# Performance work log

Hardware: AMD Instinct MI355X
Metric: run time of the kernel (lower is better)

The kernel has to match this reference:

```python
import jax, jax.numpy as jnp
import numpy as np

NX, NC = 8192, 8192
X_DIM, C_DIM, H_DIM, K_DIM, Y_DIM = 3, 3, 512, 512, 3
N_LAYERS = 4
ACTIVATION = 'sigmoid'


def _init_mlp(key, in_dim, h_dim, out_dim, n_layers):
    ks = jax.random.split(key, 3)
    W0 = jax.random.normal(ks[0], (in_dim, h_dim), jnp.float32) / np.sqrt(in_dim)
    b0 = jnp.zeros((h_dim,), jnp.float32)
    Wh = jax.random.normal(ks[1], (n_layers - 1, h_dim, h_dim), jnp.float32) / np.sqrt(h_dim)
    bh = jnp.zeros((n_layers - 1, h_dim), jnp.float32)
    Wo = jax.random.normal(ks[2], (h_dim, out_dim), jnp.float32) / np.sqrt(h_dim)
    bo = jnp.zeros((out_dim,), jnp.float32)
    return W0, b0, Wh, bh, Wo, bo


def _mlp(x, W0, b0, Wh, bh, Wo, bo):
    # SIREN-style MLP (BaseNet with x_scale=alpha=gamma=1)
    h = jnp.sin(x @ W0 + b0)
    for i in range(Wh.shape[0]):  # fixed small n_layers-1 loop
        h = jnp.sin(h @ Wh[i] + bh[i])
    return h @ Wo + bo


def setup_inputs() -> dict:
    key = jax.random.key(0)
    kx, kc, kq, kk, kv = jax.random.split(key, 5)
    inp = {
        'x': jax.random.normal(kx, (NX, X_DIM), jnp.float32),
        'c': jax.random.normal(kc, (NC, C_DIM), jnp.float32),
    }
    for name, k, in_dim, out_dim in (('Q', kq, X_DIM, K_DIM), ('K', kk, C_DIM, K_DIM), ('V', kv, C_DIM, Y_DIM)):
        W0, b0, Wh, bh, Wo, bo = _init_mlp(k, in_dim, H_DIM, out_dim, N_LAYERS)
        inp[f'{name}W0'], inp[f'{name}b0'] = W0, b0
        inp[f'{name}Wh'], inp[f'{name}bh'] = Wh, bh
        inp[f'{name}Wo'], inp[f'{name}bo'] = Wo, bo
    return inp


def reference(x, c, QW0, Qb0, QWh, Qbh, QWo, Qbo,
              KW0, Kb0, KWh, Kbh, KWo, Kbo,
              VW0, Vb0, VWh, Vbh, VWo, Vbo):
    Q = _mlp(x, QW0, Qb0, QWh, Qbh, QWo, Qbo)   # [Nx, k_dim]
    K = _mlp(c, KW0, Kb0, KWh, Kbh, KWo, Kbo)   # [Nc, k_dim]
    V = _mlp(c, VW0, Vb0, VWh, Vbh, VWo, Vbo)   # [Nc, y_dim]
    A = Q @ K.T                                  # [Nx, Nc]
    if ACTIVATION == 'sigmoid':
        A = jax.nn.sigmoid(A)
    elif ACTIVATION == 'softplus':
        A = jax.nn.softplus(A)
    elif ACTIVATION == 'softmax':
        A = jax.nn.softmax(A, axis=1)
    return A @ V                                 # [Nx, y_dim]
```

## Files before the change

### kernel.cpp

```cpp
#include <hip/hip_runtime.h>
#include <math.h>

#define NXR 8192
#define NCR 8192
#define HD  512
#define NSL 16
#define JC  (NCR / NSL)
#define KSTR 520

typedef short s16x8 __attribute__((ext_vector_type(8)));
typedef float f32x4 __attribute__((ext_vector_type(4)));
typedef unsigned short u16;

struct P11 { const float* p[11]; };
struct P3  { const float* p[3]; };

__device__ inline u16 f2bf(float f) {
    unsigned int u = __float_as_uint(f);
    u = (u + 0x7FFFu + ((u >> 16) & 1u)) >> 16;
    return (u16)u;
}
__device__ inline float bf2f(u16 h) {
    return __uint_as_float(((unsigned int)h) << 16);
}

__global__ __launch_bounds__(256) void transpose_w_all(
    P11 srcs, u16* __restrict__ out)
{
    const float* in = srcs.p[blockIdx.z];
    u16* o = out + (size_t)blockIdx.z * HD * HD;
    __shared__ float tile[32][33];
    int bx = blockIdx.x * 32, by = blockIdx.y * 32;
    int tx = threadIdx.x & 31, ty = threadIdx.x >> 5;
    for (int r = ty; r < 32; r += 8)
        tile[r][tx] = in[(size_t)(by + r) * HD + bx + tx];
    __syncthreads();
    for (int r = ty; r < 32; r += 8)
        o[(size_t)(bx + r) * HD + by + tx] = f2bf(tile[tx][r]);
}

__global__ __launch_bounds__(256) void layer0_all(
    const float* __restrict__ x, const float* __restrict__ c,
    P3 W0p, P3 b0p, u16* __restrict__ H, int net_base)
{
    int z = blockIdx.z;
    int net = net_base + z;
    const float* X  = (net == 0) ? x : c;
    const float* W0 = W0p.p[z];
    const float* b0 = b0p.p[z];
    u16* Hn = H + (size_t)z * NXR * HD;

    int idx = (blockIdx.x * 256 + threadIdx.x) * 8;
    int n = idx & (HD - 1);
    int row = idx >> 9;
    float x0 = X[row * 3 + 0], x1 = X[row * 3 + 1], x2 = X[row * 3 + 2];
    s16x8 o;
#pragma unroll
    for (int j = 0; j < 8; ++j) {
        float v = x0 * W0[n + j] + x1 * W0[HD + n + j] + x2 * W0[2 * HD + n + j] + b0[n + j];
        ((u16*)&o)[j] = f2bf(__sinf(v));
    }
    *(s16x8*)&Hn[idx] = o;
}

template<int ACT>
__global__ __launch_bounds__(256) void gemm_rs(
    const u16* __restrict__ Abase, const u16* __restrict__ Wt0, size_t wstride,
    P3 bias, u16* __restrict__ Cbase)
{
    __shared__ u16 Ws[32 * KSTR];

    const int net = blockIdx.z;
    const u16* A  = Abase + (size_t)net * NXR * HD;
    const u16* Wt = Wt0 + (size_t)net * wstride;
    const float* bias_p = bias.p[net];
    u16* C = Cbase + (size_t)net * NXR * HD;

    const int tid = threadIdx.x;
    const int wave = tid >> 6, lane = tid & 63;
    const int row0 = blockIdx.x * 128;
    const int colbase = blockIdx.y * 128;

    const int qm = lane & 15;
    const int g  = lane >> 4;

    s16x8 qf[16][2];
    {
        const u16* ap = A + (size_t)(row0 + wave * 32 + qm) * HD + g * 8;
#pragma unroll
        for (int t = 0; t < 16; ++t) {
            qf[t][0] = *(const s16x8*)(ap + t * 32);
            qf[t][1] = *(const s16x8*)(ap + (size_t)16 * HD + t * 32);
        }
    }

    for (int ct = 0; ct < 4; ++ct) {
        const int col0 = colbase + ct * 32;

#pragma unroll
        for (int i = 0; i < 8; ++i) {
            int chunk = i * 256 + tid;
            int cc = chunk >> 6;
            int ch = chunk & 63;
            s16x8 v = *(const s16x8*)(Wt + (size_t)(col0 + cc) * HD + ch * 8);
            *(s16x8*)&Ws[cc * KSTR + ch * 8] = v;
        }
        __syncthreads();

        f32x4 acc[2][2] = {};
#pragma unroll
        for (int kt = 0; kt < 16; ++kt) {
            s16x8 b0 = *(const s16x8*)&Ws[qm * KSTR + kt * 32 + g * 8];
            s16x8 b1 = *(const s16x8*)&Ws[(16 + qm) * KSTR + kt * 32 + g * 8];
            acc[0][0] = __builtin_amdgcn_mfma_f32_16x16x32_bf16(qf[kt][0], b0, acc[0][0], 0, 0, 0);
            acc[0][1] = __builtin_amdgcn_mfma_f32_16x16x32_bf16(qf[kt][0], b1, acc[0][1], 0, 0, 0);
            acc[1][0] = __builtin_amdgcn_mfma_f32_16x16x32_bf16(qf[kt][1], b0, acc[1][0], 0, 0, 0);
            acc[1][1] = __builtin_amdgcn_mfma_f32_16x16x32_bf16(qf[kt][1], b1, acc[1][1], 0, 0, 0);
        }

        float bv0 = bias_p[col0 + qm];
        float bv1 = bias_p[col0 + 16 + qm];
#pragma unroll
        for (int h = 0; h < 2; ++h) {
#pragma unroll
            for (int r = 0; r < 4; ++r) {
                int grow = row0 + wave * 32 + h * 16 + g * 4 + r;
                float v0 = acc[h][0][r] + bv0;
                float v1 = acc[h][1][r] + bv1;
                if (ACT) { v0 = __sinf(v0); v1 = __sinf(v1); }
                C[(size_t)grow * HD + col0 + qm]      = f2bf(v0);
                C[(size_t)grow * HD + col0 + 16 + qm] = f2bf(v1);
            }
        }
        __syncthreads();
    }
}

__global__ __launch_bounds__(256) void vout_k(
    const u16* __restrict__ H, const float* __restrict__ Wo,
    const float* __restrict__ bo, float* __restrict__ V)
{
    int wave = threadIdx.x >> 6, lane = threadIdx.x & 63;
    int row = blockIdx.x * 4 + wave;
    s16x8 hv = *(const s16x8*)(H + (size_t)row * HD + lane * 8);
    float a0 = 0, a1 = 0, a2 = 0;
#pragma unroll
    for (int j = 0; j < 8; ++j) {
        float hf = bf2f(((const u16*)&hv)[j]);
        int k = lane * 8 + j;
        a0 += hf * Wo[k * 3 + 0];
        a1 += hf * Wo[k * 3 + 1];
        a2 += hf * Wo[k * 3 + 2];
    }
#pragma unroll
    for (int d = 32; d >= 1; d >>= 1) {
        a0 += __shfl_down(a0, d);
        a1 += __shfl_down(a1, d);
        a2 += __shfl_down(a2, d);
    }
    if (lane == 0) {
        V[row * 3 + 0] = a0 + bo[0];
        V[row * 3 + 1] = a1 + bo[1];
        V[row * 3 + 2] = a2 + bo[2];
    }
}

__global__ __launch_bounds__(256) void attn_mfma(
    const u16* __restrict__ Q, const u16* __restrict__ K,
    const float* __restrict__ V, float* __restrict__ out)
{
    __shared__ u16 Ks[32 * KSTR];

    const int tid = threadIdx.x;
    const int wave = tid >> 6, lane = tid & 63;
    const int row0 = blockIdx.y * 128;
    const int col_base = blockIdx.x * JC;

    const int qm = lane & 15;
    const int g  = lane >> 4;

    s16x8 qf[16][2];
    {
        const u16* qp = Q + (size_t)(row0 + wave * 32 + qm) * HD + g * 8;
#pragma unroll
        for (int t = 0; t < 16; ++t) {
            qf[t][0] = *(const s16x8*)(qp + t * 32);
            qf[t][1] = *(const s16x8*)(qp + (size_t)16 * HD + t * 32);
        }
    }

    float po[2][4][3] = {};

    for (int jt = 0; jt < JC / 32; ++jt) {
        const int col0 = col_base + jt * 32;

#pragma unroll
        for (int i = 0; i < 8; ++i) {
            int chunk = i * 256 + tid;
            int cc = chunk >> 6;
            int ch = chunk & 63;
            s16x8 v = *(const s16x8*)(K + (size_t)(col0 + cc) * HD + ch * 8);
            *(s16x8*)&Ks[cc * KSTR + ch * 8] = v;
        }
        __syncthreads();

        float vv[2][3];
#pragma unroll
        for (int ct = 0; ct < 2; ++ct) {
            size_t vr = (size_t)(col0 + ct * 16 + qm) * 3;
            vv[ct][0] = V[vr + 0];
            vv[ct][1] = V[vr + 1];
            vv[ct][2] = V[vr + 2];
        }

        f32x4 acc[2][2] = {};
#pragma unroll
        for (int kt = 0; kt < 16; ++kt) {
            s16x8 b0 = *(const s16x8*)&Ks[qm * KSTR + kt * 32 + g * 8];
            s16x8 b1 = *(const s16x8*)&Ks[(16 + qm) * KSTR + kt * 32 + g * 8];
            acc[0][0] = __builtin_amdgcn_mfma_f32_16x16x32_bf16(qf[kt][0], b0, acc[0][0], 0, 0, 0);
            acc[0][1] = __builtin_amdgcn_mfma_f32_16x16x32_bf16(qf[kt][0], b1, acc[0][1], 0, 0, 0);
            acc[1][0] = __builtin_amdgcn_mfma_f32_16x16x32_bf16(qf[kt][1], b0, acc[1][0], 0, 0, 0);
            acc[1][1] = __builtin_amdgcn_mfma_f32_16x16x32_bf16(qf[kt][1], b1, acc[1][1], 0, 0, 0);
        }

#pragma unroll
        for (int h = 0; h < 2; ++h)
#pragma unroll
            for (int ct = 0; ct < 2; ++ct)
#pragma unroll
                for (int r = 0; r < 4; ++r) {
                    float s = __builtin_amdgcn_rcpf(1.f + __expf(-acc[h][ct][r]));
                    po[h][r][0] += s * vv[ct][0];
                    po[h][r][1] += s * vv[ct][1];
                    po[h][r][2] += s * vv[ct][2];
                }
        __syncthreads();
    }

#pragma unroll
    for (int h = 0; h < 2; ++h)
#pragma unroll
        for (int r = 0; r < 4; ++r)
#pragma unroll
            for (int c = 0; c < 3; ++c) {
                float v = po[h][r][c];
                v += __shfl_down(v, 8, 16);
                v += __shfl_down(v, 4, 16);
                v += __shfl_down(v, 2, 16);
                v += __shfl_down(v, 1, 16);
                if (qm == 0)
                    atomicAdd(&out[(size_t)(row0 + wave * 32 + h * 16 + g * 4 + r) * 3 + c], v);
            }
}

extern "C" void kernel_launch(void* const* d_in, const int* in_sizes, int n_in,
                              void* d_out, int out_size, void* d_ws, size_t ws_size,
                              hipStream_t stream)
{
    const float* x   = (const float*)d_in[0];
    const float* c   = (const float*)d_in[1];
    const float* QW0 = (const float*)d_in[2];
    const float* Qb0 = (const float*)d_in[3];
    const float* QWh = (const float*)d_in[4];
    const float* Qbh = (const float*)d_in[5];
    const float* QWo = (const float*)d_in[6];
    const float* Qbo = (const float*)d_in[7];
    const float* KW0 = (const float*)d_in[8];
    const float* Kb0 = (const float*)d_in[9];
    const float* KWh = (const float*)d_in[10];
    const float* Kbh = (const float*)d_in[11];
    const float* KWo = (const float*)d_in[12];
    const float* Kbo = (const float*)d_in[13];
    const float* VW0 = (const float*)d_in[14];
    const float* Vb0 = (const float*)d_in[15];
    const float* VWh = (const float*)d_in[16];
    const float* Vbh = (const float*)d_in[17];
    const float* VWo = (const float*)d_in[18];
    const float* Vbo = (const float*)d_in[19];

    char* ws = (char*)d_ws;
    const size_t WTN = (size_t)HD * HD;
    const size_t MB = 1048576;
    const size_t NET = (size_t)NXR * HD;

    u16* wT = (u16*)ws;
    P11 tsrc;
    for (int l = 0; l < 3; ++l) {
        tsrc.p[l * 3 + 0] = QWh + (size_t)l * WTN;
        tsrc.p[l * 3 + 1] = KWh + (size_t)l * WTN;
        tsrc.p[l * 3 + 2] = VWh + (size_t)l * WTN;
    }
    tsrc.p[9]  = QWo;
    tsrc.p[10] = KWo;
    transpose_w_all<<<dim3(16, 16, 11), 256, 0, stream>>>(tsrc, wT);

    const int L0G = NXR * HD / 2048;
    const u16* Qb; const u16* Kb; const float* Vf;

    if (ws_size >= 57 * MB) {
        u16*   hA = (u16*)(ws + 6 * MB);
        u16*   hB = (u16*)(ws + 30 * MB);
        float* Vff = (float*)(ws + 54 * MB);

        P3 w0 = {{QW0, KW0, VW0}}, b0 = {{Qb0, Kb0, Vb0}};
        layer0_all<<<dim3(L0G, 1, 3), 256, 0, stream>>>(x, c, w0, b0, hA, 0);

        dim3 g3(NXR / 128, HD / 128, 3);
        {
            P3 b = {{Qbh + 0 * HD, Kbh + 0 * HD, Vbh + 0 * HD}};
            gemm_rs<1><<<g3, 256, 0, stream>>>(hA, wT + 0 * 3 * WTN, WTN, b, hB);
        }
        {
            P3 b = {{Qbh + 1 * HD, Kbh + 1 * HD, Vbh + 1 * HD}};
            gemm_rs<1><<<g3, 256, 0, stream>>>(hB, wT + 1 * 3 * WTN, WTN, b, hA);
        }
        {
            P3 b = {{Qbh + 2 * HD, Kbh + 2 * HD, Vbh + 2 * HD}};
            gemm_rs<1><<<g3, 256, 0, stream>>>(hA, wT + 2 * 3 * WTN, WTN, b, hB);
        }
        {
            P3 b = {{Qbo, Kbo, nullptr}};
            gemm_rs<0><<<dim3(NXR / 128, HD / 128, 2), 256, 0, stream>>>(
                hB, wT + 9 * WTN, WTN, b, hA);
        }
        vout_k<<<NCR / 4, 256, 0, stream>>>(hB + 2 * NET, VWo, Vbo, Vff);

        Qb = hA; Kb = hA + NET; Vf = Vff;
    } else {
        u16*   R1 = (u16*)(ws + 6 * MB);
        u16*   R2 = (u16*)(ws + 22 * MB);
        float* Vff = (float*)(ws + 38 * MB);

        {
            P3 w0 = {{VW0, nullptr, nullptr}}, b0 = {{Vb0, nullptr, nullptr}};
            layer0_all<<<dim3(L0G, 1, 1), 256, 0, stream>>>(x, c, w0, b0, R1, 2);
        }
        dim3 gv(NXR / 128, HD / 128, 1);
        {
            P3 b = {{Vbh + 0 * HD, nullptr, nullptr}};
            gemm_rs<1><<<gv, 256, 0, stream>>>(R1, wT + (0 * 3 + 2) * WTN, 0, b, R2);
        }
        {
            P3 b = {{Vbh + 1 * HD, nullptr, nullptr}};
            gemm_rs<1><<<gv, 256, 0, stream>>>(R2, wT + (1 * 3 + 2) * WTN, 0, b, R1);
        }
        {
            P3 b = {{Vbh + 2 * HD, nullptr, nullptr}};
            gemm_rs<1><<<gv, 256, 0, stream>>>(R1, wT + (2 * 3 + 2) * WTN, 0, b, R2);
        }
        vout_k<<<NCR / 4, 256, 0, stream>>>(R2, VWo, Vbo, Vff);

        {
            P3 w0 = {{QW0, KW0, nullptr}}, b0 = {{Qb0, Kb0, nullptr}};
            layer0_all<<<dim3(L0G, 1, 2), 256, 0, stream>>>(x, c, w0, b0, R1, 0);
        }
        dim3 gqk(NXR / 128, HD / 128, 2);
        {
            P3 b = {{Qbh + 0 * HD, Kbh + 0 * HD, nullptr}};
            gemm_rs<1><<<gqk, 256, 0, stream>>>(R1, wT + 0 * 3 * WTN, WTN, b, R2);
        }
        {
            P3 b = {{Qbh + 1 * HD, Kbh + 1 * HD, nullptr}};
            gemm_rs<1><<<gqk, 256, 0, stream>>>(R2, wT + 1 * 3 * WTN, WTN, b, R1);
        }
        {
            P3 b = {{Qbh + 2 * HD, Kbh + 2 * HD, nullptr}};
            gemm_rs<1><<<gqk, 256, 0, stream>>>(R1, wT + 2 * 3 * WTN, WTN, b, R2);
        }
        {
            P3 b = {{Qbo, Kbo, nullptr}};
            gemm_rs<0><<<gqk, 256, 0, stream>>>(R2, wT + 9 * WTN, WTN, b, R1);
        }
        Qb = R1; Kb = R1 + NET; Vf = Vff;
    }

    hipMemsetAsync(d_out, 0, (size_t)out_size * sizeof(float), stream);
    attn_mfma<<<dim3(NSL, NXR / 128), 256, 0, stream>>>(Qb, Kb, Vf, (float*)d_out);
}
```

Measured before the change: 306.3 us.

## Register-prefetch next weight/K tile and halve attention column slices

Both the MLP GEMM and the attention kernel now load the next 32-column tile of weights or K into registers while the MFMA loop runs on the current tile held in shared memory. The barrier placement is reorganised so there is one barrier before the shared-memory store and one after it, which hides global-load latency behind compute. NSL drops from 16 to 8, giving each attention block twice as many columns and halving the number of atomic adds, at the cost of fewer blocks in the grid. The prefetch adds 8 vector registers per thread on top of the already large qf fragment array, which risks lower occupancy or register spills.

```diff
diff --git a/kernel.cpp b/kernel.cpp
--- a/kernel.cpp
+++ b/kernel.cpp
@@ -4,7 +4,7 @@
 #define NXR 8192
 #define NCR 8192
 #define HD  512
-#define NSL 16
+#define NSL 8
 #define JC  (NCR / NSL)
 #define KSTR 520
 
@@ -84,6 +84,13 @@
     const int qm = lane & 15;
     const int g  = lane >> 4;
 
+    s16x8 pre[8];
+#pragma unroll
+    for (int i = 0; i < 8; ++i) {
+        int chunk = i * 256 + tid;
+        pre[i] = *(const s16x8*)(Wt + (size_t)(colbase + (chunk >> 6)) * HD + (chunk & 63) * 8);
+    }
+
     s16x8 qf[16][2];
     {
         const u16* ap = A + (size_t)(row0 + wave * 32 + qm) * HD + g * 8;
@@ -97,15 +104,22 @@
     for (int ct = 0; ct < 4; ++ct) {
         const int col0 = colbase + ct * 32;
 
+        __syncthreads();
 #pragma unroll
         for (int i = 0; i < 8; ++i) {
             int chunk = i * 256 + tid;
-            int cc = chunk >> 6;
-            int ch = chunk & 63;
-            s16x8 v = *(const s16x8*)(Wt + (size_t)(col0 + cc) * HD + ch * 8);
-            *(s16x8*)&Ws[cc * KSTR + ch * 8] = v;
+            *(s16x8*)&Ws[(chunk >> 6) * KSTR + (chunk & 63) * 8] = pre[i];
         }
         __syncthreads();
+
+        if (ct + 1 < 4) {
+            const int ncol = colbase + (ct + 1) * 32;
+#pragma unroll
+            for (int i = 0; i < 8; ++i) {
+                int chunk = i * 256 + tid;
+                pre[i] = *(const s16x8*)(Wt + (size_t)(ncol + (chunk >> 6)) * HD + (chunk & 63) * 8);
+            }
+        }
 
         f32x4 acc[2][2] = {};
 #pragma unroll
@@ -132,7 +146,6 @@
                 C[(size_t)grow * HD + col0 + 16 + qm] = f2bf(v1);
             }
         }
-        __syncthreads();
     }
 }
 
@@ -179,6 +192,13 @@
     const int qm = lane & 15;
     const int g  = lane >> 4;
 
+    s16x8 pre[8];
+#pragma unroll
+    for (int i = 0; i < 8; ++i) {
+        int chunk = i * 256 + tid;
+        pre[i] = *(const s16x8*)(K + (size_t)(col_base + (chunk >> 6)) * HD + (chunk & 63) * 8);
+    }
+
     s16x8 qf[16][2];
     {
         const u16* qp = Q + (size_t)(row0 + wave * 32 + qm) * HD + g * 8;
@@ -194,15 +214,22 @@
     for (int jt = 0; jt < JC / 32; ++jt) {
         const int col0 = col_base + jt * 32;
 
+        __syncthreads();
 #pragma unroll
         for (int i = 0; i < 8; ++i) {
             int chunk = i * 256 + tid;
-            int cc = chunk >> 6;
-            int ch = chunk & 63;
-            s16x8 v = *(const s16x8*)(K + (size_t)(col0 + cc) * HD + ch * 8);
-            *(s16x8*)&Ks[cc * KSTR + ch * 8] = v;
+            *(s16x8*)&Ks[(chunk >> 6) * KSTR + (chunk & 63) * 8] = pre[i];
         }
         __syncthreads();
+
+        if (jt + 1 < JC / 32) {
+            const int ncol = col_base + (jt + 1) * 32;
+#pragma unroll
+            for (int i = 0; i < 8; ++i) {
+                int chunk = i * 256 + tid;
+                pre[i] = *(const s16x8*)(K + (size_t)(ncol + (chunk >> 6)) * HD + (chunk & 63) * 8);
+            }
+        }
 
         float vv[2][3];
 #pragma unroll
@@ -235,7 +262,6 @@
                     po[h][r][1] += s * vv[ct][1];
                     po[h][r][2] += s * vv[ct][2];
                 }
-        __syncthreads();
     }
 
 #pragma unroll
```

Measured after the change: 293.3 us. 4.2% less time.

## Fuse hidden MLP layers and V projection into one persistent in-place kernel

Applied to the files above, without the earlier changes.

Replaces the per-layer gemm_rs launches and the separate vout_k kernel with a single mlp_mega kernel. Each block owns a 128-row strip of one network and runs every hidden layer in place, reloading its rows from global memory between layers. The V network's final 3-wide projection is done inside the same kernel. The attention column split (NSL) is also halved and the low-workspace fallback path is dropped. This saves launches and inter-kernel round trips, but cuts the MLP grid from 768 to 192 blocks, so each block does far more serial work and fewer CUs may be busy.

```diff
diff --git a/kernel.cpp b/kernel.cpp
--- a/kernel.cpp
+++ b/kernel.cpp
@@ -4,7 +4,7 @@
 #define NXR 8192
 #define NCR 8192
 #define HD  512
-#define NSL 16
+#define NSL 8
 #define JC  (NCR / NSL)
 #define KSTR 520
 
@@ -14,6 +14,7 @@
 
 struct P11 { const float* p[11]; };
 struct P3  { const float* p[3]; };
+struct MB12 { const float* p[12]; };
 
 __device__ inline u16 f2bf(float f) {
     unsigned int u = __float_as_uint(f);
@@ -41,11 +42,10 @@
 
 __global__ __launch_bounds__(256) void layer0_all(
     const float* __restrict__ x, const float* __restrict__ c,
-    P3 W0p, P3 b0p, u16* __restrict__ H, int net_base)
+    P3 W0p, P3 b0p, u16* __restrict__ H)
 {
     int z = blockIdx.z;
-    int net = net_base + z;
-    const float* X  = (net == 0) ? x : c;
+    const float* X  = (z == 0) ? x : c;
     const float* W0 = W0p.p[z];
     const float* b0 = b0p.p[z];
     u16* Hn = H + (size_t)z * NXR * HD;
@@ -63,105 +63,120 @@
     *(s16x8*)&Hn[idx] = o;
 }
 
-template<int ACT>
-__global__ __launch_bounds__(256) void gemm_rs(
-    const u16* __restrict__ Abase, const u16* __restrict__ Wt0, size_t wstride,
-    P3 bias, u16* __restrict__ Cbase)
+__global__ __launch_bounds__(256) void mlp_mega(
+    u16* __restrict__ h, const u16* __restrict__ wT,
+    MB12 mb, const float* __restrict__ VWo, float* __restrict__ Vf)
 {
     __shared__ u16 Ws[32 * KSTR];
-
+    __shared__ float VWs[HD * 3];
+
+    const size_t WTN = (size_t)HD * HD;
     const int net = blockIdx.z;
-    const u16* A  = Abase + (size_t)net * NXR * HD;
-    const u16* Wt = Wt0 + (size_t)net * wstride;
-    const float* bias_p = bias.p[net];
-    u16* C = Cbase + (size_t)net * NXR * HD;
-
     const int tid = threadIdx.x;
     const int wave = tid >> 6, lane = tid & 63;
     const int row0 = blockIdx.x * 128;
-    const int colbase = blockIdx.y * 128;
+    u16* strip = h + (size_t)net * NXR * HD;
 
     const int qm = lane & 15;
     const int g  = lane >> 4;
 
+    const int nlayers = (net == 2) ? 3 : 4;
+
     s16x8 qf[16][2];
-    {
-        const u16* ap = A + (size_t)(row0 + wave * 32 + qm) * HD + g * 8;
-#pragma unroll
-        for (int t = 0; t < 16; ++t) {
-            qf[t][0] = *(const s16x8*)(ap + t * 32);
-            qf[t][1] = *(const s16x8*)(ap + (size_t)16 * HD + t * 32);
-        }
-    }
-
-    for (int ct = 0; ct < 4; ++ct) {
-        const int col0 = colbase + ct * 32;
-
-#pragma unroll
-        for (int i = 0; i < 8; ++i) {
-            int chunk = i * 256 + tid;
-            int cc = chunk >> 6;
-            int ch = chunk & 63;
-            s16x8 v = *(const s16x8*)(Wt + (size_t)(col0 + cc) * HD + ch * 8);
-            *(s16x8*)&Ws[cc * KSTR + ch * 8] = v;
-        }
+
+    for (int layer = 0; layer < nlayers; ++layer) {
+        const u16* Wt = (layer < 3) ? wT + (size_t)(layer * 3 + net) * WTN
+                                    : wT + (size_t)(9 + net) * WTN;
+        const float* bias_p = mb.p[(layer < 3) ? layer * 3 + net : 9 + net];
+        const int act = (layer < 3);
+
+        {
+            const u16* ap = strip + (size_t)(row0 + wave * 32 + qm) * HD + g * 8;
+#pragma unroll
+            for (int t = 0; t < 16; ++t) {
+                qf[t][0] = *(const s16x8*)(ap + t * 32);
+                qf[t][1] = *(const s16x8*)(ap + (size_t)16 * HD + t * 32);
+            }
+        }
+
+        for (int ct = 0; ct < 16; ++ct) {
+            const int col0 = ct * 32;
+
+#pragma unroll
+            for (int i = 0; i < 8; ++i) {
+                int chunk = i * 256 + tid;
+                int cc = chunk >> 6, ch = chunk & 63;
+                s16x8 v = *(const s16x8*)(Wt + (size_t)(col0 + cc) * HD + ch * 8);
+                *(s16x8*)&Ws[cc * KSTR + ch * 8] = v;
+            }
+            __syncthreads();
+
+            f32x4 acc[2][2] = {};
+#pragma unroll
+            for (int kt = 0; kt < 16; ++kt) {
+                s16x8 b0 = *(const s16x8*)&Ws[qm * KSTR + kt * 32 + g * 8];
+                s16x8 b1 = *(const s16x8*)&Ws[(16 + qm) * KSTR + kt * 32 + g * 8];
+                acc[0][0] = __builtin_amdgcn_mfma_f32_16x16x32_bf16(qf[kt][0], b0, acc[0][0], 0, 0, 0);
+                acc[0][1] = __builtin_amdgcn_mfma_f32_16x16x32_bf16(qf[kt][0], b1, acc[0][1], 0, 0, 0);
+                acc[1][0] = __builtin_amdgcn_mfma_f32_16x16x32_bf16(qf[kt][1], b0, acc[1][0], 0, 0, 0);
+                acc[1][1] = __builtin_amdgcn_mfma_f32_16x16x32_bf16(qf[kt][1], b1, acc[1][1], 0, 0, 0);
+            }
+
+            float bv0 = bias_p[col0 + qm];
+            float bv1 = bias_p[col0 + 16 + qm];
+#pragma unroll
+            for (int hh = 0; hh < 2; ++hh) {
+#pragma unroll
+                for (int r = 0; r < 4; ++r) {
+                    int grow = row0 + wave * 32 + hh * 16 + g * 4 + r;
+                    float v0 = acc[hh][0][r] + bv0;
+                    float v1 = acc[hh][1][r] + bv1;
+                    if (act) { v0 = __sinf(v0); v1 = __sinf(v1); }
+                    strip[(size_t)grow * HD + col0 + qm]      = f2bf(v0);
+                    strip[(size_t)grow * HD + col0 + 16 + qm] = f2bf(v1);
+                }
+            }
+            __syncthreads();
+        }
+        __threadfence();
+    }
+
+    if (net == 2) {
+        {
+            const u16* ap = strip + (size_t)(row0 + wave * 32 + qm) * HD + g * 8;
+#pragma unroll
+            for (int t = 0; t < 16; ++t) {
+                qf[t][0] = *(const s16x8*)(ap + t * 32);
+                qf[t][1] = *(const s16x8*)(ap + (size_t)16 * HD + t * 32);
+            }
+        }
+        for (int i = tid; i < HD * 3; i += 256) VWs[i] = VWo[i];
         __syncthreads();
-
-        f32x4 acc[2][2] = {};
-#pragma unroll
-        for (int kt = 0; kt < 16; ++kt) {
-            s16x8 b0 = *(const s16x8*)&Ws[qm * KSTR + kt * 32 + g * 8];
-            s16x8 b1 = *(const s16x8*)&Ws[(16 + qm) * KSTR + kt * 32 + g * 8];
-            acc[0][0] = __builtin_amdgcn_mfma_f32_16x16x32_bf16(qf[kt][0], b0, acc[0][0], 0, 0, 0);
-            acc[0][1] = __builtin_amdgcn_mfma_f32_16x16x32_bf16(qf[kt][0], b1, acc[0][1], 0, 0, 0);
-            acc[1][0] = __builtin_amdgcn_mfma_f32_16x16x32_bf16(qf[kt][1], b0, acc[1][0], 0, 0, 0);
-            acc[1][1] = __builtin_amdgcn_mfma_f32_16x16x32_bf16(qf[kt][1], b1, acc[1][1], 0, 0, 0);
-        }
-
-        float bv0 = bias_p[col0 + qm];
-        float bv1 = bias_p[col0 + 16 + qm];
-#pragma unroll
-        for (int h = 0; h < 2; ++h) {
-#pragma unroll
-            for (int r = 0; r < 4; ++r) {
-                int grow = row0 + wave * 32 + h * 16 + g * 4 + r;
-                float v0 = acc[h][0][r] + bv0;
-                float v1 = acc[h][1][r] + bv1;
-                if (ACT) { v0 = __sinf(v0); v1 = __sinf(v1); }
-                C[(size_t)grow * HD + col0 + qm]      = f2bf(v0);
-                C[(size_t)grow * HD + col0 + 16 + qm] = f2bf(v1);
-            }
-        }
-        __syncthreads();
-    }
-}
-
-__global__ __launch_bounds__(256) void vout_k(
-    const u16* __restrict__ H, const float* __restrict__ Wo,
-    const float* __restrict__ bo, float* __restrict__ V)
-{
-    int wave = threadIdx.x >> 6, lane = threadIdx.x & 63;
-    int row = blockIdx.x * 4 + wave;
-    s16x8 hv = *(const s16x8*)(H + (size_t)row * HD + lane * 8);
-    float a0 = 0, a1 = 0, a2 = 0;
-#pragma unroll
-    for (int j = 0; j < 8; ++j) {
-        float hf = bf2f(((const u16*)&hv)[j]);
-        int k = lane * 8 + j;
-        a0 += hf * Wo[k * 3 + 0];
-        a1 += hf * Wo[k * 3 + 1];
-        a2 += hf * Wo[k * 3 + 2];
-    }
-#pragma unroll
-    for (int d = 32; d >= 1; d >>= 1) {
-        a0 += __shfl_down(a0, d);
-        a1 += __shfl_down(a1, d);
-        a2 += __shfl_down(a2, d);
-    }
-    if (lane == 0) {
-        V[row * 3 + 0] = a0 + bo[0];
-        V[row * 3 + 1] = a1 + bo[1];
-        V[row * 3 + 2] = a2 + bo[2];
+        const float* Vbo = mb.p[11];
+
+        float o[2][3] = {};
+#pragma unroll
+        for (int t = 0; t < 16; ++t)
+#pragma unroll
+            for (int hh = 0; hh < 2; ++hh)
+#pragma unroll
+                for (int j = 0; j < 8; ++j) {
+                    float a = bf2f(((const u16*)&qf[t][hh])[j]);
+                    int k = t * 32 + g * 8 + j;
+                    o[hh][0] += a * VWs[k * 3 + 0];
+                    o[hh][1] += a * VWs[k * 3 + 1];
+                    o[hh][2] += a * VWs[k * 3 + 2];
+                }
+#pragma unroll
+        for (int hh = 0; hh < 2; ++hh)
+#pragma unroll
+            for (int cc = 0; cc < 3; ++cc) {
+                float v = o[hh][cc];
+                v += __shfl_down(v, 32);
+                v += __shfl_down(v, 16);
+                if (g == 0)
+                    Vf[(size_t)(row0 + wave * 32 + hh * 16 + qm) * 3 + cc] = v + Vbo[cc];
+            }
     }
 }
 
@@ -281,10 +296,12 @@
 
     char* ws = (char*)d_ws;
     const size_t WTN = (size_t)HD * HD;
-    const size_t MB = 1048576;
     const size_t NET = (size_t)NXR * HD;
 
-    u16* wT = (u16*)ws;
+    u16*   wT = (u16*)ws;
+    u16*   hA = (u16*)(ws + 11 * WTN * sizeof(u16));
+    float* Vf = (float*)(ws + 11 * WTN * sizeof(u16) + 3 * NET * sizeof(u16));
+
     P11 tsrc;
     for (int l = 0; l < 3; ++l) {
         tsrc.p[l * 3 + 0] = QWh + (size_t)l * WTN;
@@ -295,86 +312,25 @@
     tsrc.p[10] = KWo;
     transpose_w_all<<<dim3(16, 16, 11), 256, 0, stream>>>(tsrc, wT);
 
-    const int L0G = NXR * HD / 2048;
-    const u16* Qb; const u16* Kb; const float* Vf;
-
-    if (ws_size >= 57 * MB) {
-        u16*   hA = (u16*)(ws + 6 * MB);
-        u16*   hB = (u16*)(ws + 30 * MB);
-        float* Vff = (float*)(ws + 54 * MB);
-
+    {
         P3 w0 = {{QW0, KW0, VW0}}, b0 = {{Qb0, Kb0, Vb0}};
-        layer0_all<<<dim3(L0G, 1, 3), 256, 0, stream>>>(x, c, w0, b0, hA, 0);
-
-        dim3 g3(NXR / 128, HD / 128, 3);
-        {
-            P3 b = {{Qbh + 0 * HD, Kbh + 0 * HD, Vbh + 0 * HD}};
-            gemm_rs<1><<<g3, 256, 0, stream>>>(hA, wT + 0 * 3 * WTN, WTN, b, hB);
-        }
-        {
-            P3 b = {{Qbh + 1 * HD, Kbh + 1 * HD, Vbh + 1 * HD}};
-            gemm_rs<1><<<g3, 256, 0, stream>>>(hB, wT + 1 * 3 * WTN, WTN, b, hA);
-        }
-        {
-            P3 b = {{Qbh + 2 * HD, Kbh + 2 * HD, Vbh + 2 * HD}};
-            gemm_rs<1><<<g3, 256, 0, stream>>>(hA, wT + 2 * 3 * WTN, WTN, b, hB);
-        }
-        {
-            P3 b = {{Qbo, Kbo, nullptr}};
-            gemm_rs<0><<<dim3(NXR / 128, HD / 128, 2), 256, 0, stream>>>(
-                hB, wT + 9 * WTN, WTN, b, hA);
-        }
-        vout_k<<<NCR / 4, 256, 0, stream>>>(hB + 2 * NET, VWo, Vbo, Vff);
-
-        Qb = hA; Kb = hA + NET; Vf = Vff;
-    } else {
-        u16*   R1 = (u16*)(ws + 6 * MB);
-        u16*   R2 = (u16*)(ws + 22 * MB);
-        float* Vff = (float*)(ws + 38 * MB);
-
-        {
-            P3 w0 = {{VW0, nullptr, nullptr}}, b0 = {{Vb0, nullptr, nullptr}};
-            layer0_all<<<dim3(L0G, 1, 1), 256, 0, stream>>>(x, c, w0, b0, R1, 2);
-        }
-        dim3 gv(NXR / 128, HD / 128, 1);
-        {
-            P3 b = {{Vbh + 0 * HD, nullptr, nullptr}};
-            gemm_rs<1><<<gv, 256, 0, stream>>>(R1, wT + (0 * 3 + 2) * WTN, 0, b, R2);
-        }
-        {
-            P3 b = {{Vbh + 1 * HD, nullptr, nullptr}};
-            gemm_rs<1><<<gv, 256, 0, stream>>>(R2, wT + (1 * 3 + 2) * WTN, 0, b, R1);
-        }
-        {
-            P3 b = {{Vbh + 2 * HD, nullptr, nullptr}};
-            gemm_rs<1><<<gv, 256, 0, stream>>>(R1, wT + (2 * 3 + 2) * WTN, 0, b, R2);
-        }
-        vout_k<<<NCR / 4, 256, 0, stream>>>(R2, VWo, Vbo, Vff);
-
-        {
-            P3 w0 = {{QW0, KW0, nullptr}}, b0 = {{Qb0, Kb0, nullptr}};
-            layer0_all<<<dim3(L0G, 1, 2), 256, 0, stream>>>(x, c, w0, b0, R1, 0);
-        }
-        dim3 gqk(NXR / 128, HD / 128, 2);
-        {
-            P3 b = {{Qbh + 0 * HD, Kbh + 0 * HD, nullptr}};
-            gemm_rs<1><<<gqk, 256, 0, stream>>>(R1, wT + 0 * 3 * WTN, WTN, b, R2);
-        }
-        {
-            P3 b = {{Qbh + 1 * HD, Kbh + 1 * HD, nullptr}};
-            gemm_rs<1><<<gqk, 256, 0, stream>>>(R2, wT + 1 * 3 * WTN, WTN, b, R1);
-        }
-        {
-            P3 b = {{Qbh + 2 * HD, Kbh + 2 * HD, nullptr}};
-            gemm_rs<1><<<gqk, 256, 0, stream>>>(R1, wT + 2 * 3 * WTN, WTN, b, R2);
-        }
-        {
-            P3 b = {{Qbo, Kbo, nullptr}};
-            gemm_rs<0><<<gqk, 256, 0, stream>>>(R2, wT + 9 * WTN, WTN, b, R1);
-        }
-        Qb = R1; Kb = R1 + NET; Vf = Vff;
+        layer0_all<<<dim3(NXR * HD / 2048, 1, 3), 256, 0, stream>>>(x, c, w0, b0, hA);
+    }
+
+    {
+        MB12 mb;
+        for (int l = 0; l < 3; ++l) {
+            mb.p[l * 3 + 0] = Qbh + (size_t)l * HD;
+            mb.p[l * 3 + 1] = Kbh + (size_t)l * HD;
+            mb.p[l * 3 + 2] = Vbh + (size_t)l * HD;
+        }
+        mb.p[9]  = Qbo;
+        mb.p[10] = Kbo;
+        mb.p[11] = Vbo;
+        mlp_mega<<<dim3(NXR / 128, 1, 3), 256, 0, stream>>>(hA, wT, mb, VWo, Vf);
     }
 
     hipMemsetAsync(d_out, 0, (size_t)out_size * sizeof(float), stream);
-    attn_mfma<<<dim3(NSL, NXR / 128), 256, 0, stream>>>(Qb, Kb, Vf, (float*)d_out);
-}
+    attn_mfma<<<dim3(NSL, NXR / 128), 256, 0, stream>>>(
+        hA, hA + NET, Vf, (float*)d_out);
+}
```

After: 484.2 us. 58.1% more time.
